# Kernel optimization log

Hardware: AMD Instinct MI355X
Metric: run time of the kernel (lower is better)

Reference implementation:

```python
import jax, jax.numpy as jnp
import numpy as np

B, CIN, H, W = 8, 256, 96, 96
EMB1, EMB2 = 256, 128
NCLS, NEG, NLAY = 80, 3, 3
SIGMA, BETA, NEG_SCOPE = 0.5, 0.3, 2.0


def setup_inputs() -> dict:
    key = jax.random.key(0)
    ks = jax.random.split(key, 8)
    s = 0.01
    return {
        "x": jax.random.normal(ks[0], (B, CIN, H, W), jnp.float32),
        "conv1_w": jax.random.normal(ks[1], (EMB1, CIN, 3, 3), jnp.float32) * s,
        "conv1_b": jnp.zeros((EMB1,), jnp.float32),
        "bn_gamma": jnp.ones((EMB1,), jnp.float32),
        "bn_beta": jnp.zeros((EMB1,), jnp.float32),
        "bn_mean": jnp.zeros((EMB1,), jnp.float32),
        "bn_var": jnp.ones((EMB1,), jnp.float32),
        "conv2_w": jax.random.normal(ks[2], (EMB2, EMB1, 3, 3), jnp.float32) * s,
        "conv2_b": jnp.zeros((EMB2,), jnp.float32),
        "rep_w": jax.random.normal(ks[3], (NCLS * EMB2, 1), jnp.float32) * s,
        "rep_b": jax.random.normal(ks[4], (NCLS * EMB2,), jnp.float32) * s,
        "neg_w": jax.random.normal(ks[5], (NEG, NLAY, EMB2, EMB2), jnp.float32) * s,
        "neg_b": jnp.zeros((NEG, NLAY, EMB2), jnp.float32),
    }


def _conv3(x, w, b):
    # 3x3, stride 1, padding 1 (SAME)
    y = jax.lax.conv_general_dilated(
        x, w, window_strides=(1, 1), padding="SAME",
        dimension_numbers=("NCHW", "OIHW", "NCHW"))
    return y + b[None, :, None, None]


def _l2norm(v, axis):
    return v / jnp.maximum(jnp.linalg.norm(v, axis=axis, keepdims=True), 1e-12)


def reference(x, conv1_w, conv1_b, bn_gamma, bn_beta, bn_mean, bn_var,
              conv2_w, conv2_b, rep_w, rep_b, neg_w, neg_b):
    # --- emb_module: Conv-BN-Conv, then L2 normalize channels ---
    h = _conv3(x, conv1_w, conv1_b)
    scale = bn_gamma / jnp.sqrt(bn_var + 1e-5)
    h = (h - bn_mean[None, :, None, None]) * scale[None, :, None, None] + bn_beta[None, :, None, None]
    emb = _conv3(h, conv2_w, conv2_b)          # [B, E, H, W]
    emb = _l2norm(emb, axis=1)

    # --- positive prototypes: rep_fc(1.0) -> [C, 1, E], normalized ---
    reps = (rep_w[:, 0] + rep_b).reshape(NCLS, 1, EMB2)
    reps = _l2norm(reps, axis=2)               # [C, 1, E]
    r = reps[:, 0]                              # [C, E]

    # --- negative prototypes: 3 MPCs (Linear-ReLU-Linear-ReLU-Linear) ---
    def mpc(Ws, bs):                            # Ws [NLAY,E,E], bs [NLAY,E]
        hh = r
        for i in range(NLAY):
            hh = hh @ Ws[i].T + bs[i]
            if i < NLAY - 1:
                hh = jax.nn.relu(hh)
        return hh                               # [C, E]
    reps_neg = jax.vmap(mpc)(neg_w, neg_b)      # [NEG, C, E]
    reps_neg = jnp.transpose(reps_neg, (1, 0, 2))  # [C, NEG, E]
    reps_neg = _l2norm(reps_neg, axis=2)

    # --- L2 distances; both sides unit-norm so ||e-r||^2 = 2 - 2 e.r ---
    dot = jnp.einsum("behw,cme->bcmhw", emb, reps)       # [B,C,1,H,W]
    distances = jnp.sqrt(jnp.maximum(2.0 - 2.0 * dot, 0.0))
    dot_n = jnp.einsum("behw,cme->bcmhw", emb, reps_neg)  # [B,C,NEG,H,W]
    distances_neg = jnp.sqrt(jnp.maximum(2.0 - 2.0 * dot_n, 0.0))

    inv2s2 = 1.0 / (2.0 * SIGMA ** 2)
    probs_neg = jnp.exp(-distances_neg ** 2 * inv2s2)
    cls_score_neg = probs_neg.max(axis=2)                 # [B,C,H,W]
    probs_ori = jnp.exp(-distances ** 2 * inv2s2).max(axis=2)

    min_neg = distances_neg.min(axis=2, keepdims=True)    # [B,C,1,H,W]
    shifted = distances + BETA * jax.nn.relu(NEG_SCOPE - min_neg)
    probs = jnp.exp(-shifted ** 2 * inv2s2)
    cls_score = probs.max(axis=2)                         # [B,C,H,W]

    # forward_single applies inverse_sigmoid to cls_score
    eps = 1e-5
    cs = jnp.clip(cls_score, 0.0, 1.0)
    cls_score = jnp.log(jnp.clip(cs, eps, None) / jnp.clip(1.0 - cs, eps, None))

    return (cls_score, cls_score_neg, distances, distances_neg, probs_ori)
```

## Files before the change

### kernel.cpp

```cpp
#include <hip/hip_runtime.h>
#include <cstddef>
#include <cstdint>

constexpr int Bz = 8, CIN = 256, Hh = 96, Ww = 96;
constexpr int EMB1 = 256, EMB2 = 128, NCLS = 80;
constexpr int HP = 98;
constexpr size_t PIX = (size_t)Hh * Ww;
constexpr size_t XP_ELEMS = (size_t)Bz * HP * HP * CIN;

constexpr size_t O0 = 0;
constexpr size_t O1 = (size_t)Bz * NCLS * PIX;
constexpr size_t O2 = 2 * O1;
constexpr size_t O3 = 3 * O1;
constexpr size_t O4 = 6 * O1;

typedef short bf16x8 __attribute__((ext_vector_type(8)));
typedef float f32x4 __attribute__((ext_vector_type(4)));

__device__ inline unsigned short f2bf(float f) {
  union { float f; unsigned int u; } v; v.f = f;
  unsigned int r = v.u + 0x7fffu + ((v.u >> 16) & 1u);
  return (unsigned short)(r >> 16);
}

#define GLD16(gp, lp)                                              \
  __builtin_amdgcn_global_load_lds(                                \
      (__attribute__((address_space(1))) void*)((void*)(gp)),      \
      (__attribute__((address_space(3))) void*)(lp), 16, 0, 0)

__global__ __launch_bounds__(256) void pad_x_kernel(const float* __restrict__ x,
                                                    unsigned short* __restrict__ xp) {
  const int p = blockIdx.x;
  const int b = blockIdx.y;
  const int ic = threadIdx.x;
  const int y = p / HP, xx = p % HP;
  float v = 0.f;
  if (y >= 1 && y <= Hh && xx >= 1 && xx <= Ww)
    v = x[(((size_t)b * CIN + ic) * Hh + (y - 1)) * Ww + (xx - 1)];
  xp[((size_t)b * (HP * HP) + p) * CIN + ic] = f2bf(v);
}

__global__ __launch_bounds__(256) void prep_w_kernel(
    const float* __restrict__ w1, const float* __restrict__ w2,
    const float* __restrict__ c1b, const float* __restrict__ g,
    const float* __restrict__ be, const float* __restrict__ mu,
    const float* __restrict__ var, unsigned short* __restrict__ wt1,
    unsigned short* __restrict__ wt2, float* __restrict__ bns,
    float* __restrict__ bno) {
  const int idx = blockIdx.x * 256 + threadIdx.x;
  if (idx < 9 * 256 * 256) {
    const int ic = idx & 255, oc = (idx >> 8) & 255, tap = idx >> 16;
    wt1[idx] = f2bf(w1[((size_t)(oc * 256 + ic)) * 9 + tap]);
  }
  if (idx < 9 * 128 * 256) {
    const int ic = idx & 255, oc = (idx >> 8) & 127, tap = idx >> 15;
    wt2[idx] = f2bf(w2[((size_t)(oc * 256 + ic)) * 9 + tap]);
  }
  if (idx < 256) {
    const float s = g[idx] * rsqrtf(var[idx] + 1e-5f);
    bns[idx] = s;
    bno[idx] = (c1b[idx] - mu[idx]) * s + be[idx];
  }
}

__global__ __launch_bounds__(128) void rep_norm_kernel(const float* __restrict__ rw,
                                                       const float* __restrict__ rb,
                                                       float* __restrict__ r,
                                                       unsigned short* __restrict__ Rb) {
  __shared__ float red[2];
  const int c = blockIdx.x, t = threadIdx.x;
  const float v = rw[c * 128 + t] + rb[c * 128 + t];
  float s = v * v;
  for (int msk = 1; msk < 64; msk <<= 1) s += __shfl_xor(s, msk, 64);
  if ((t & 63) == 0) red[t >> 6] = s;
  __syncthreads();
  const float ss = red[0] + red[1];
  const float rn = 1.f / fmaxf(sqrtf(ss), 1e-12f);
  r[c * 128 + t] = v * rn;
  Rb[(size_t)(c * 4) * 128 + t] = f2bf(v * rn);
}

__global__ __launch_bounds__(128) void mlp_neg_kernel(const float* __restrict__ r,
                                                      const float* __restrict__ W,
                                                      const float* __restrict__ bb,
                                                      unsigned short* __restrict__ Rb) {
  __shared__ float h0[128], h1[128];
  __shared__ float red[2];
  const int c = blockIdx.x, ng = blockIdx.y, t = threadIdx.x;
  h0[t] = r[c * 128 + t];
  __syncthreads();
  float s = 0.f;
  for (int lay = 0; lay < 3; ++lay) {
    const float* hin = (lay & 1) ? h1 : h0;
    float* hout = (lay & 1) ? h0 : h1;
    const float* wr = W + (((size_t)ng * 3 + lay) * 128 + t) * 128;
    s = bb[(ng * 3 + lay) * 128 + t];
    for (int e = 0; e < 128; ++e) s += wr[e] * hin[e];
    if (lay < 2) hout[t] = fmaxf(s, 0.f);
    __syncthreads();
  }
  float q = s * s;
  for (int msk = 1; msk < 64; msk <<= 1) q += __shfl_xor(q, msk, 64);
  if ((t & 63) == 0) red[t >> 6] = q;
  __syncthreads();
  const float ss = red[0] + red[1];
  const float rn = 1.f / fmaxf(sqrtf(ss), 1e-12f);
  Rb[((size_t)(c * 4) + 1 + ng) * 128 + t] = f2bf(s * rn);
}

template <int OC, bool BN>
__global__ __launch_bounds__(256) void conv3x3_mfma(
    const unsigned short* __restrict__ in, const unsigned short* __restrict__ wt,
    const float* __restrict__ e0, const float* __restrict__ e1,
    unsigned short* __restrict__ out16) {
  __shared__ unsigned short smA[128 * 32];
  __shared__ unsigned short smB[128 * 32];
  __shared__ float nrm[128][2];
  const int tile = blockIdx.x;
  const int oc0 = blockIdx.y * 128;
  const int b = blockIdx.z;
  const int ty = (tile / 6) * 8, tx = (tile % 6) * 16;
  const int t = threadIdx.x;
  const int lane = t & 63, w = t >> 6;
  const int wm = w & 1, wn = w >> 1;
  const int quad = lane >> 4, col = lane & 15;
  const int chl = (lane & 3) * 8;

  int rowA[2], colA[2], ocB[2];
#pragma unroll
  for (int i = 0; i < 2; ++i) {
    const int px = (w * 2 + i) * 16 + (lane >> 2);
    rowA[i] = ty + (px >> 4);
    colA[i] = tx + (px & 15);
    ocB[i] = oc0 + (w * 2 + i) * 16 + (lane >> 2);
  }

  f32x4 acc[4][4];
#pragma unroll
  for (int mt = 0; mt < 4; ++mt)
#pragma unroll
    for (int nt = 0; nt < 4; ++nt) acc[mt][nt] = {0.f, 0.f, 0.f, 0.f};

  for (int tap = 0; tap < 9; ++tap) {
    const int ky = tap / 3, kx = tap % 3;
    const unsigned short* aB[2];
    const unsigned short* bB[2];
#pragma unroll
    for (int i = 0; i < 2; ++i) {
      aB[i] = in + (((size_t)b * HP + rowA[i] + ky) * HP + colA[i] + kx) * 256 + chl;
      bB[i] = wt + ((size_t)(tap * OC + ocB[i])) * 256 + chl;
    }
    for (int ch0 = 0; ch0 < 256; ch0 += 32) {
      __syncthreads();
      GLD16(aB[0] + ch0, (char*)smA + (w * 2 + 0) * 1024);
      GLD16(aB[1] + ch0, (char*)smA + (w * 2 + 1) * 1024);
      GLD16(bB[0] + ch0, (char*)smB + (w * 2 + 0) * 1024);
      GLD16(bB[1] + ch0, (char*)smB + (w * 2 + 1) * 1024);
      __syncthreads();
      bf16x8 af[4], bf[4];
#pragma unroll
      for (int mt = 0; mt < 4; ++mt)
        af[mt] = *(const bf16x8*)((const char*)smA +
                                  (wm * 64 + mt * 16 + col) * 64 + quad * 16);
#pragma unroll
      for (int nt = 0; nt < 4; ++nt)
        bf[nt] = *(const bf16x8*)((const char*)smB +
                                  (wn * 64 + nt * 16 + col) * 64 + quad * 16);
#pragma unroll
      for (int mt = 0; mt < 4; ++mt)
#pragma unroll
        for (int nt = 0; nt < 4; ++nt)
          acc[mt][nt] = __builtin_amdgcn_mfma_f32_16x16x32_bf16(
              af[mt], bf[nt], acc[mt][nt], 0, 0, 0);
    }
  }

  float sc[4], of[4];
#pragma unroll
  for (int nt = 0; nt < 4; ++nt) {
    const int oc = oc0 + wn * 64 + nt * 16 + col;
    sc[nt] = e0[oc];
    of[nt] = BN ? e1[oc] : 0.f;
  }
  if (BN) {
#pragma unroll
    for (int mt = 0; mt < 4; ++mt)
#pragma unroll
      for (int r = 0; r < 4; ++r) {
        const int px = wm * 64 + mt * 16 + quad * 4 + r;
        const int y = ty + (px >> 4), x = tx + (px & 15);
        unsigned short* rowp =
            out16 + (((size_t)b * HP + y + 1) * HP + x + 1) * 256 + oc0 + wn * 64 + col;
#pragma unroll
        for (int nt = 0; nt < 4; ++nt)
          rowp[nt * 16] = f2bf(acc[mt][nt][r] * sc[nt] + of[nt]);
      }
  } else {
    float part[4][4];
#pragma unroll
    for (int mt = 0; mt < 4; ++mt)
#pragma unroll
      for (int r = 0; r < 4; ++r) {
        float s = 0.f;
#pragma unroll
        for (int nt = 0; nt < 4; ++nt) {
          const float v = acc[mt][nt][r] + sc[nt];
          s += v * v;
        }
        part[mt][r] = s;
      }
#pragma unroll
    for (int msk = 1; msk < 16; msk <<= 1)
#pragma unroll
      for (int mt = 0; mt < 4; ++mt)
#pragma unroll
        for (int r = 0; r < 4; ++r)
          part[mt][r] += __shfl_xor(part[mt][r], msk, 64);
    if (col == 0) {
#pragma unroll
      for (int mt = 0; mt < 4; ++mt)
#pragma unroll
        for (int r = 0; r < 4; ++r)
          nrm[wm * 64 + mt * 16 + quad * 4 + r][wn] = part[mt][r];
    }
    __syncthreads();
#pragma unroll
    for (int mt = 0; mt < 4; ++mt)
#pragma unroll
      for (int r = 0; r < 4; ++r) {
        const int px = wm * 64 + mt * 16 + quad * 4 + r;
        const int y = ty + (px >> 4), x = tx + (px & 15);
        const float nn = nrm[px][0] + nrm[px][1];
        const float rn = 1.f / fmaxf(sqrtf(nn), 1e-12f);
        unsigned short* rowp =
            out16 + (((size_t)b * Hh + y) * Ww + x) * 128 + wn * 64 + col;
#pragma unroll
        for (int nt = 0; nt < 4; ++nt)
          rowp[nt * 16] = f2bf((acc[mt][nt][r] + sc[nt]) * rn);
      }
  }
}

__device__ inline void xpose4(float& r0, float& r1, float& r2, float& r3,
                              int lane) {
  const int b1 = (lane >> 1) & 1, b0 = lane & 1;
  float s0 = b1 ? r0 : r2;
  float s1 = b1 ? r1 : r3;
  s0 = __shfl_xor(s0, 2, 64);
  s1 = __shfl_xor(s1, 2, 64);
  if (b1) { r0 = s0; r1 = s1; } else { r2 = s0; r3 = s1; }
  float t0 = b0 ? r0 : r1;
  float t1 = b0 ? r2 : r3;
  t0 = __shfl_xor(t0, 1, 64);
  t1 = __shfl_xor(t1, 1, 64);
  if (b0) { r0 = t0; r2 = t1; } else { r1 = t0; r3 = t1; }
}

__global__ __launch_bounds__(256) void score_mfma(
    const unsigned short* __restrict__ embb, const unsigned short* __restrict__ Rb,
    float* __restrict__ out) {
  const int px0 = blockIdx.x * 64;
  const int b = blockIdx.y;
  const int t = threadIdx.x;
  const int lane = t & 63, w = t >> 6;
  const int quad = lane >> 4, col = lane & 15;
  const int n0 = w * 80;
  const unsigned short* Abase = embb + ((size_t)b * PIX + px0) * 128;

  f32x4 acc[4][5];
#pragma unroll
  for (int mt = 0; mt < 4; ++mt)
#pragma unroll
    for (int nt = 0; nt < 5; ++nt) acc[mt][nt] = {0.f, 0.f, 0.f, 0.f};

#pragma unroll
  for (int ks = 0; ks < 4; ++ks) {
    bf16x8 bf[5], af[4];
#pragma unroll
    for (int nt = 0; nt < 5; ++nt)
      bf[nt] = *(const bf16x8*)(Rb + (size_t)(n0 + nt * 16 + col) * 128 +
                                ks * 32 + quad * 8);
#pragma unroll
    for (int mt = 0; mt < 4; ++mt)
      af[mt] = *(const bf16x8*)(Abase + (size_t)(mt * 16 + col) * 128 +
                                ks * 32 + quad * 8);
#pragma unroll
    for (int mt = 0; mt < 4; ++mt)
#pragma unroll
      for (int nt = 0; nt < 5; ++nt)
        acc[mt][nt] = __builtin_amdgcn_mfma_f32_16x16x32_bf16(
            af[mt], bf[nt], acc[mt][nt], 0, 0, 0);
  }

  const int j = lane & 3, kq = (lane >> 2) & 3;
#pragma unroll
  for (int mt = 0; mt < 4; ++mt) {
    const int px = px0 + mt * 16 + quad * 4 + j;
#pragma unroll
    for (int nt = 0; nt < 5; ++nt) {
      float v0 = acc[mt][nt][0], v1 = acc[mt][nt][1];
      float v2 = acc[mt][nt][2], v3 = acc[mt][nt][3];
      xpose4(v0, v1, v2, v3, lane);
      const int gc = w * 20 + nt * 4 + kq;
      const float d2p = fmaxf(2.f - 2.f * v0, 0.f);
      const float dist = sqrtf(d2p);
      const float q0 = fmaxf(2.f - 2.f * v1, 0.f);
      const float q1 = fmaxf(2.f - 2.f * v2, 0.f);
      const float q2 = fmaxf(2.f - 2.f * v3, 0.f);
      const float dn0 = sqrtf(q0), dn1 = sqrtf(q1), dn2 = sqrtf(q2);
      const float pn = __expf(-2.f * fminf(q0, fminf(q1, q2)));
      const float pori = __expf(-2.f * d2p);
      const float minn = fminf(dn0, fminf(dn1, dn2));
      const float shifted = dist + 0.3f * fmaxf(2.0f - minn, 0.f);
      const float p = __expf(-2.f * shifted * shifted);
      const float clsv = __logf(fmaxf(p, 1e-5f) / fmaxf(1.f - p, 1e-5f));
      const size_t bc = ((size_t)b * NCLS + gc) * PIX + px;
      out[O0 + bc] = clsv;
      out[O1 + bc] = pn;
      out[O2 + bc] = dist;
      out[O4 + bc] = pori;
      const size_t b3 = (((size_t)b * NCLS + gc) * 3) * PIX + px;
      out[O3 + b3] = dn0;
      out[O3 + b3 + PIX] = dn1;
      out[O3 + b3 + 2 * PIX] = dn2;
    }
  }
}

extern "C" void kernel_launch(void* const* d_in, const int* in_sizes, int n_in,
                              void* d_out, int out_size, void* d_ws,
                              size_t ws_size, hipStream_t stream) {
  const float* x = (const float*)d_in[0];
  const float* w1 = (const float*)d_in[1];
  const float* c1b = (const float*)d_in[2];
  const float* g = (const float*)d_in[3];
  const float* be = (const float*)d_in[4];
  const float* mu = (const float*)d_in[5];
  const float* var = (const float*)d_in[6];
  const float* w2 = (const float*)d_in[7];
  const float* c2b = (const float*)d_in[8];
  const float* rw = (const float*)d_in[9];
  const float* rb = (const float*)d_in[10];
  const float* nw = (const float*)d_in[11];
  const float* nb = (const float*)d_in[12];
  float* out = (float*)d_out;

  unsigned short* xp = (unsigned short*)d_ws;
  unsigned short* hp = xp + XP_ELEMS;
  unsigned short* wt1 = hp + XP_ELEMS;
  unsigned short* wt2 = wt1 + 589824;
  float* bns = (float*)(wt2 + 294912);
  float* bno = bns + 256;
  float* rpv = bno + 256;
  unsigned short* Rb = (unsigned short*)(rpv + 10240);
  unsigned short* embb = xp;

  hipMemsetAsync(hp, 0, XP_ELEMS * sizeof(unsigned short), stream);
  pad_x_kernel<<<dim3(HP * HP, Bz), 256, 0, stream>>>(x, xp);
  prep_w_kernel<<<2304, 256, 0, stream>>>(w1, w2, c1b, g, be, mu, var, wt1, wt2,
                                          bns, bno);
  rep_norm_kernel<<<NCLS, 128, 0, stream>>>(rw, rb, rpv, Rb);
  mlp_neg_kernel<<<dim3(NCLS, 3), 128, 0, stream>>>(rpv, nw, nb, Rb);
  conv3x3_mfma<256, true><<<dim3(72, 2, Bz), 256, 0, stream>>>(xp, wt1, bns,
                                                               bno, hp);
  conv3x3_mfma<128, false><<<dim3(72, 1, Bz), 256, 0, stream>>>(hp, wt2, c2b,
                                                                nullptr, embb);
  score_mfma<<<dim3(144, Bz), 256, 0, stream>>>(embb, Rb, out);
}
```

Baseline: 574.7 us.

## Double-buffer conv LDS loads and transpose input padding through shared memory

The conv MFMA kernel now flattens its tap/channel loops into 72 stages and double-buffers the A and B LDS tiles. The next stage's global-to-LDS loads are issued before the current stage's MFMAs, with one barrier per stage instead of two, so load latency can overlap compute. Separately, the NCHW-to-padded-NHWC bf16 conversion now goes through a shared-memory tile so both the reads and the writes are coalesced. The padding border is now set by an extra memset of the whole buffer. The cost is twice the LDS and an additional full-buffer memset.

```diff
diff --git a/kernel.cpp b/kernel.cpp
--- a/kernel.cpp
+++ b/kernel.cpp
@@ -30,14 +30,20 @@
 
 __global__ __launch_bounds__(256) void pad_x_kernel(const float* __restrict__ x,
                                                     unsigned short* __restrict__ xp) {
-  const int p = blockIdx.x;
-  const int b = blockIdx.y;
-  const int ic = threadIdx.x;
-  const int y = p / HP, xx = p % HP;
-  float v = 0.f;
-  if (y >= 1 && y <= Hh && xx >= 1 && xx <= Ww)
-    v = x[(((size_t)b * CIN + ic) * Hh + (y - 1)) * Ww + (xx - 1)];
-  xp[((size_t)b * (HP * HP) + p) * CIN + ic] = f2bf(v);
+  __shared__ float tile[32][257];
+  const int b = blockIdx.z, y = blockIdx.y, x0 = blockIdx.x * 32;
+  const int t = threadIdx.x;
+  const int px = t & 31, cg = t >> 5;
+  const float* src = x + (((size_t)b * CIN) * Hh + y) * Ww + x0 + px;
+#pragma unroll 4
+  for (int c = cg; c < CIN; c += 8)
+    tile[px][c] = src[(size_t)c * Hh * Ww];
+  __syncthreads();
+  unsigned short* orow =
+      xp + (((size_t)b * HP + y + 1) * HP + (x0 + 1)) * 256 + t;
+#pragma unroll 4
+  for (int p = 0; p < 32; ++p)
+    orow[(size_t)p * 256] = f2bf(tile[p][t]);
 }
 
 __global__ __launch_bounds__(256) void prep_w_kernel(
@@ -113,8 +119,8 @@
     const unsigned short* __restrict__ in, const unsigned short* __restrict__ wt,
     const float* __restrict__ e0, const float* __restrict__ e1,
     unsigned short* __restrict__ out16) {
-  __shared__ unsigned short smA[128 * 32];
-  __shared__ unsigned short smB[128 * 32];
+  __shared__ unsigned short smA[2][128 * 32];
+  __shared__ unsigned short smB[2][128 * 32];
   __shared__ float nrm[128][2];
   const int tile = blockIdx.x;
   const int oc0 = blockIdx.y * 128;
@@ -126,13 +132,15 @@
   const int quad = lane >> 4, col = lane & 15;
   const int chl = (lane & 3) * 8;
 
-  int rowA[2], colA[2], ocB[2];
+  size_t baseA[2], baseB[2];
 #pragma unroll
   for (int i = 0; i < 2; ++i) {
     const int px = (w * 2 + i) * 16 + (lane >> 2);
-    rowA[i] = ty + (px >> 4);
-    colA[i] = tx + (px & 15);
-    ocB[i] = oc0 + (w * 2 + i) * 16 + (lane >> 2);
+    const int rowA = ty + (px >> 4);
+    const int colA = tx + (px & 15);
+    const int ocB = oc0 + (w * 2 + i) * 16 + (lane >> 2);
+    baseA[i] = (((size_t)b * HP + rowA) * HP + colA) * 256 + chl;
+    baseB[i] = (size_t)ocB * 256 + chl;
   }
 
   f32x4 acc[4][4];
@@ -141,38 +149,41 @@
 #pragma unroll
     for (int nt = 0; nt < 4; ++nt) acc[mt][nt] = {0.f, 0.f, 0.f, 0.f};
 
-  for (int tap = 0; tap < 9; ++tap) {
-    const int ky = tap / 3, kx = tap % 3;
-    const unsigned short* aB[2];
-    const unsigned short* bB[2];
-#pragma unroll
-    for (int i = 0; i < 2; ++i) {
-      aB[i] = in + (((size_t)b * HP + rowA[i] + ky) * HP + colA[i] + kx) * 256 + chl;
-      bB[i] = wt + ((size_t)(tap * OC + ocB[i])) * 256 + chl;
-    }
-    for (int ch0 = 0; ch0 < 256; ch0 += 32) {
-      __syncthreads();
-      GLD16(aB[0] + ch0, (char*)smA + (w * 2 + 0) * 1024);
-      GLD16(aB[1] + ch0, (char*)smA + (w * 2 + 1) * 1024);
-      GLD16(bB[0] + ch0, (char*)smB + (w * 2 + 0) * 1024);
-      GLD16(bB[1] + ch0, (char*)smB + (w * 2 + 1) * 1024);
-      __syncthreads();
-      bf16x8 af[4], bf[4];
-#pragma unroll
-      for (int mt = 0; mt < 4; ++mt)
-        af[mt] = *(const bf16x8*)((const char*)smA +
-                                  (wm * 64 + mt * 16 + col) * 64 + quad * 16);
+  auto stage = [&](int s, int buf) {
+    const int tap = s >> 3;
+    const int ch0 = (s & 7) << 5;
+    const int sA = ((tap / 3) * HP + (tap % 3)) * 256 + ch0;
+    const int sB = tap * (OC * 256) + ch0;
+    char* dA = (char*)smA[buf];
+    char* dB = (char*)smB[buf];
+    GLD16(in + baseA[0] + sA, dA + (w * 2 + 0) * 1024);
+    GLD16(in + baseA[1] + sA, dA + (w * 2 + 1) * 1024);
+    GLD16(wt + baseB[0] + sB, dB + (w * 2 + 0) * 1024);
+    GLD16(wt + baseB[1] + sB, dB + (w * 2 + 1) * 1024);
+  };
+
+  stage(0, 0);
+  __syncthreads();
+  int cur = 0;
+  for (int s = 0; s < 72; ++s) {
+    if (s < 71) stage(s + 1, cur ^ 1);
+    bf16x8 af[4], bf[4];
+#pragma unroll
+    for (int mt = 0; mt < 4; ++mt)
+      af[mt] = *(const bf16x8*)((const char*)smA[cur] +
+                                (wm * 64 + mt * 16 + col) * 64 + quad * 16);
+#pragma unroll
+    for (int nt = 0; nt < 4; ++nt)
+      bf[nt] = *(const bf16x8*)((const char*)smB[cur] +
+                                (wn * 64 + nt * 16 + col) * 64 + quad * 16);
+#pragma unroll
+    for (int mt = 0; mt < 4; ++mt)
 #pragma unroll
       for (int nt = 0; nt < 4; ++nt)
-        bf[nt] = *(const bf16x8*)((const char*)smB +
-                                  (wn * 64 + nt * 16 + col) * 64 + quad * 16);
-#pragma unroll
-      for (int mt = 0; mt < 4; ++mt)
-#pragma unroll
-        for (int nt = 0; nt < 4; ++nt)
-          acc[mt][nt] = __builtin_amdgcn_mfma_f32_16x16x32_bf16(
-              af[mt], bf[nt], acc[mt][nt], 0, 0, 0);
-    }
+        acc[mt][nt] = __builtin_amdgcn_mfma_f32_16x16x32_bf16(
+            af[mt], bf[nt], acc[mt][nt], 0, 0, 0);
+    __syncthreads();
+    cur ^= 1;
   }
 
   float sc[4], of[4];
@@ -355,8 +366,9 @@
   unsigned short* Rb = (unsigned short*)(rpv + 10240);
   unsigned short* embb = xp;
 
+  hipMemsetAsync(xp, 0, XP_ELEMS * sizeof(unsigned short), stream);
   hipMemsetAsync(hp, 0, XP_ELEMS * sizeof(unsigned short), stream);
-  pad_x_kernel<<<dim3(HP * HP, Bz), 256, 0, stream>>>(x, xp);
+  pad_x_kernel<<<dim3(3, Hh, Bz), 256, 0, stream>>>(x, xp);
   prep_w_kernel<<<2304, 256, 0, stream>>>(w1, w2, c1b, g, be, mu, var, wt1, wt2,
                                           bns, bno);
   rep_norm_kernel<<<NCLS, 128, 0, stream>>>(rw, rb, rpv, Rb);
```

Result: no change. 571.8 us (-0.5%).
